# Kernel optimization log

Hardware: AMD Instinct MI355X
Metric: run time of the kernel (lower is better)

## Reference

```python
import jax, jax.numpy as jnp
import numpy as np

NUM_HEADS = 16


def rotate_half(x):
    half = x.shape[-1] // 2
    return jnp.concatenate((-x[..., half:], x[..., :half]), axis=-1)


def rope_tables(seq_len, head_dim, dtype=jnp.float32):
    inv_freq = 1.0 / (10000.0 ** (jnp.arange(0, head_dim, 2, dtype=jnp.float32) / head_dim))
    t = jnp.arange(seq_len, dtype=jnp.float32)
    freqs = jnp.outer(t, inv_freq)                 # [S, hd/2]
    emb = jnp.concatenate((freqs, freqs), axis=-1)  # [S, hd]
    return jnp.cos(emb).astype(dtype), jnp.sin(emb).astype(dtype)


def setup_inputs() -> dict:
    key = jax.random.key(0)
    k1, k2, k3 = jax.random.split(key, 3)
    B, S, D = 2, 2048, 1024
    x = jax.random.normal(k1, (B, S, D), dtype=jnp.float32)
    # causal lower-triangular mask, broadcast over batch/heads
    mask = jnp.tril(jnp.ones((S, S), dtype=bool))[None, None, :, :]
    w_qkv = jax.random.normal(k2, (3 * D, D), dtype=jnp.float32) * (D ** -0.5)
    w_out = jax.random.normal(k3, (D, D), dtype=jnp.float32) * (D ** -0.5)
    return {"x": x, "mask": mask, "w_qkv": w_qkv, "w_out": w_out}


def reference(x, mask, w_qkv, w_out):
    B, S, D = x.shape
    H = NUM_HEADS
    hd = D // H
    scale = hd ** -0.5

    qkv = jnp.einsum('bsd,ed->bse', x, w_qkv)          # [B, S, 3D]
    q, k, v = jnp.split(qkv, 3, axis=-1)

    def split(t):
        return t.reshape(B, S, H, hd).transpose(0, 2, 1, 3)  # [B, H, S, hd]

    q, k, v = split(q), split(k), split(v)

    cos, sin = rope_tables(S, hd, x.dtype)             # [S, hd]
    cos = cos[None, None]
    sin = sin[None, None]
    q = q * cos + rotate_half(q) * sin
    k = k * cos + rotate_half(k) * sin

    attn = jnp.einsum('bhqd,bhkd->bhqk', q, k) * scale  # [B, H, S, S]
    attn = jnp.where(mask, attn, jnp.float32(-jnp.inf).astype(attn.dtype))
    attn = jax.nn.softmax(attn, axis=-1)
    out = jnp.einsum('bhqk,bhkd->bhqd', attn, v)        # [B, H, S, hd]
    out = out.transpose(0, 2, 1, 3).reshape(B, S, D)
    return jnp.einsum('bsd,ed->bse', out, w_out)
```

## Files before the change

kernel.cpp:

```cpp
#include <hip/hip_runtime.h>
#include <hip/hip_bf16.h>

typedef __attribute__((ext_vector_type(8))) __bf16 bf16x8;
typedef __attribute__((ext_vector_type(4))) __bf16 bf16x4;
typedef __attribute__((ext_vector_type(2))) __bf16 bf16x2;
typedef __attribute__((ext_vector_type(4))) float f32x4;
typedef __attribute__((ext_vector_type(16))) float f32x16;

#define SEQ 2048
#define NH 16
#define HD 64
#define DMODEL 1024
#define BATCH 2
#define MTOT 4096

__device__ __forceinline__ void gl_lds16(const void* g, void* l) {
    __builtin_amdgcn_global_load_lds(
        (const __attribute__((address_space(1))) void*)(uintptr_t)g,
        (__attribute__((address_space(3))) void*)(uintptr_t)l,
        16, 0, 0);
}

__device__ __forceinline__ unsigned pk2(float x, float y) {
    union { bf16x2 h; unsigned u; } c;
    c.h = bf16x2{ (__bf16)x, (__bf16)y };
    return c.u;
}

__global__ __launch_bounds__(256) void cast3(const float4* __restrict__ x,
                                             const float4* __restrict__ wq,
                                             const float4* __restrict__ wo,
                                             __bf16* __restrict__ xb,
                                             __bf16* __restrict__ wqb,
                                             __bf16* __restrict__ wob) {
    const int NX  = 1024 * 1024;
    const int NWQ = 768 * 1024;
    const int NTOT = NX + NWQ + 256 * 1024;
    int i = blockIdx.x * 256 + threadIdx.x;
    if (i >= NTOT) return;
    float4 v; __bf16* dst; int j;
    if (i < NX)            { j = i;            v = x[j];  dst = xb;  }
    else if (i < NX + NWQ) { j = i - NX;       v = wq[j]; dst = wqb; }
    else                   { j = i - NX - NWQ; v = wo[j]; dst = wob; }
    bf16x4 o = { (__bf16)v.x, (__bf16)v.y, (__bf16)v.z, (__bf16)v.w };
    *(bf16x4*)(dst + (size_t)j * 4) = o;
}

__global__ __launch_bounds__(256) void gemm_bt(const __bf16* __restrict__ A,
                                               const __bf16* __restrict__ Bt,
                                               __bf16* __restrict__ Cb,
                                               float* __restrict__ Cf,
                                               int M, int N, int K, int bf16out) {
    __shared__ __bf16 sA[128 * 64];
    __shared__ __bf16 sB[128 * 64];
    const int tid = threadIdx.x, lane = tid & 63, wave = tid >> 6;
    const int lrow = lane & 15, quad = lane >> 4;
    const int m0 = blockIdx.y * 128, n0 = blockIdx.x * 128;
    const int wm = wave >> 1, wn = wave & 1;

    const __bf16* ap[4]; const __bf16* bp[4]; int ldso[4];
#pragma unroll
    for (int i = 0; i < 4; ++i) {
        int r0 = i * 32 + wave * 8;
        int row = r0 + (lane >> 3);
        int cg = (lane & 7) ^ (row & 7);
        ap[i] = A + (size_t)(m0 + row) * K + cg * 8;
        bp[i] = Bt + (size_t)(n0 + row) * K + cg * 8;
        ldso[i] = r0 * 128;
    }
    int arow[4], brow[4];
#pragma unroll
    for (int i = 0; i < 4; ++i) {
        arow[i] = wm * 64 + i * 16 + lrow;
        brow[i] = wn * 64 + i * 16 + lrow;
    }

    f32x4 z = {0.f, 0.f, 0.f, 0.f};
    f32x4 acc[4][4];
#pragma unroll
    for (int i = 0; i < 4; ++i)
#pragma unroll
        for (int j = 0; j < 4; ++j) acc[i][j] = z;

    char* sAb = (char*)sA; char* sBb = (char*)sB;
    for (int k0 = 0; k0 < K; k0 += 64) {
#pragma unroll
        for (int i = 0; i < 4; ++i) gl_lds16(ap[i] + k0, sAb + ldso[i]);
#pragma unroll
        for (int i = 0; i < 4; ++i) gl_lds16(bp[i] + k0, sBb + ldso[i]);
        __syncthreads();
#pragma unroll
        for (int ks = 0; ks < 2; ++ks) {
            bf16x8 af[4], bfr[4];
#pragma unroll
            for (int i = 0; i < 4; ++i)
                af[i] = *(const bf16x8*)(sAb + arow[i] * 128 +
                                         (((ks * 4 + quad) ^ (arow[i] & 7)) << 4));
#pragma unroll
            for (int i = 0; i < 4; ++i)
                bfr[i] = *(const bf16x8*)(sBb + brow[i] * 128 +
                                          (((ks * 4 + quad) ^ (brow[i] & 7)) << 4));
#pragma unroll
            for (int i = 0; i < 4; ++i)
#pragma unroll
                for (int j = 0; j < 4; ++j)
                    acc[i][j] = __builtin_amdgcn_mfma_f32_16x16x32_bf16(
                        af[i], bfr[j], acc[i][j], 0, 0, 0);
        }
        __syncthreads();
    }
#pragma unroll
    for (int i = 0; i < 4; ++i)
#pragma unroll
        for (int j = 0; j < 4; ++j)
#pragma unroll
            for (int r = 0; r < 4; ++r) {
                int row = m0 + wm * 64 + i * 16 + quad * 4 + r;
                int col = n0 + wn * 64 + j * 16 + lrow;
                if (bf16out) Cb[(size_t)row * N + col] = (__bf16)acc[i][j][r];
                else         Cf[(size_t)row * N + col] = acc[i][j][r];
            }
}

__global__ __launch_bounds__(256) void rope_qk(const __bf16* __restrict__ qkv,
                                               __bf16* __restrict__ Qp,
                                               __bf16* __restrict__ Kp) {
    int t = blockIdx.x * 256 + threadIdx.x;
    int g = t & 3, hh = (t >> 2) & 15, isk = (t >> 6) & 1, m = t >> 7;
    int s = m & (SEQ - 1), b = m >> 11;
    const __bf16* src = qkv + (size_t)m * 3072 + isk * 1024 + hh * 64 + g * 8;
    bf16x8 v0 = *(const bf16x8*)src;
    bf16x8 v1 = *(const bf16x8*)(src + 32);
    float sf = (float)s;
    float scale = isk ? 1.0f : 0.18033688011112042f;
    float base = 0.15915494309189535f * exp2f(-(float)(g * 8) * 0.4152410118609203f);
    const float rj[8] = {1.0f, 0.7498942093324559f, 0.5623413251903491f,
                         0.4216965034285822f, 0.31622776601683794f,
                         0.23713737056616552f, 0.1778279410038923f,
                         0.13335214321633242f};
    bf16x8 o0, o1;
#pragma unroll
    for (int j = 0; j < 8; ++j) {
        float rev = sf * (base * rj[j]);
        float frac = rev - floorf(rev);
        float sn = __builtin_amdgcn_sinf(frac);
        float cs = __builtin_amdgcn_cosf(frac);
        float a = (float)v0[j], bb = (float)v1[j];
        o0[j] = (__bf16)((a * cs - bb * sn) * scale);
        o1[j] = (__bf16)((bb * cs + a * sn) * scale);
    }
    __bf16* dst = (isk ? Kp : Qp) + ((size_t)(b * NH + hh) * SEQ + s) * HD + g * 8;
    *(bf16x8*)dst = o0;
    *(bf16x8*)(dst + 32) = o1;
}

__global__ __launch_bounds__(256) void v_transpose(const __bf16* __restrict__ qkv,
                                                   __bf16* __restrict__ Vt) {
    __shared__ __bf16 t[64 * 80];
    const int tid = threadIdx.x;
    const int s0 = blockIdx.x * 64;
    const int bh = blockIdx.y;
    const int b = bh >> 4, h = bh & 15;
#pragma unroll
    for (int it = 0; it < 2; ++it) {
        int idx = tid + it * 256;
        int s = idx >> 3, c = idx & 7;
        bf16x8 v = *(const bf16x8*)(qkv + ((size_t)(b * SEQ + s0 + s)) * 3072 +
                                    2048 + h * 64 + c * 8);
#pragma unroll
        for (int j = 0; j < 8; ++j) t[s * 80 + c * 8 + j] = v[j];
    }
    __syncthreads();
    int j = tid >> 2, sc = (tid & 3) * 16;
    __align__(16) __bf16 tmp[16];
#pragma unroll
    for (int k = 0; k < 16; ++k) tmp[k] = t[(sc + k) * 80 + j];
    __bf16* dst = Vt + ((size_t)bh * HD + j) * SEQ + s0 + sc;
    *(bf16x8*)dst = *(bf16x8*)tmp;
    *(bf16x8*)(dst + 8) = *(bf16x8*)(tmp + 8);
}

__global__ __launch_bounds__(256) void flash_attn(const __bf16* __restrict__ Qp,
                                                  const __bf16* __restrict__ Kp,
                                                  const __bf16* __restrict__ Vtp,
                                                  __bf16* __restrict__ Aout) {
    __shared__ __bf16 sK[128 * 64];
    __shared__ __bf16 sV[2][64 * 64];

    const int tid = threadIdx.x, lane = tid & 63, wave = tid >> 6;
    const int ql = lane & 31, half = lane >> 5;
    const int bh = blockIdx.x;
    const int qt = 15 - blockIdx.y;
    const int b = bh >> 4, hh = bh & 15;
    const int q0 = qt * 128;
    const int qrow = q0 + wave * 32 + ql;

    bf16x8 qf[4];
    const __bf16* qb = Qp + ((size_t)bh * SEQ + qrow) * HD + half * 8;
#pragma unroll
    for (int kc = 0; kc < 4; ++kc) qf[kc] = *(const bf16x8*)(qb + kc * 16);

    const __bf16* kp[4]; int kldso[4];
    const __bf16* vp[4]; int vldso[4];
#pragma unroll
    for (int i = 0; i < 4; ++i) {
        int r0 = i * 32 + wave * 8;
        int row = r0 + (lane >> 3);
        int cg = (lane & 7) ^ (row & 7);
        kp[i] = Kp + ((size_t)bh * SEQ + row) * HD + cg * 8;
        kldso[i] = r0 * 128;
        int s = i >> 1;
        int rv0 = (i & 1) * 32 + wave * 8;
        int vrow = rv0 + (lane >> 3);
        int vcg = (lane & 7) ^ (vrow & 7);
        vp[i] = Vtp + ((size_t)bh * HD + vrow) * SEQ + s * 64 + vcg * 8;
        vldso[i] = s * 8192 + rv0 * 128;
    }

    char* sKb = (char*)sK;
    char* sVb = (char*)sV;

    f32x16 zz = {0.f};
    f32x16 o0 = zz, o1 = zz;
    float l = 0.f;

    const int nkt = qt + 1;
    for (int kt = 0; kt < nkt; ++kt) {
        const int k0 = kt * 128;
#pragma unroll
        for (int i = 0; i < 4; ++i) gl_lds16(kp[i] + (size_t)k0 * HD, sKb + kldso[i]);
#pragma unroll
        for (int i = 0; i < 4; ++i) gl_lds16(vp[i] + k0, sVb + vldso[i]);
        __syncthreads();

        const bool diag = (kt == nkt - 1);
#pragma unroll
        for (int ktl = 0; ktl < 4; ++ktl) {
            int keyl = ktl * 32 + ql;
            f32x16 st = zz;
#pragma unroll
            for (int kc = 0; kc < 4; ++kc) {
                bf16x8 kf = *(const bf16x8*)(
                    sKb + keyl * 128 + (((kc * 2 + half) ^ (keyl & 7)) << 4));
                st = __builtin_amdgcn_mfma_f32_32x32x16_bf16(kf, qf[kc], st, 0, 0, 0);
            }

#pragma unroll
            for (int g = 0; g < 4; ++g)
#pragma unroll
                for (int t = 0; t < 4; ++t) {
                    float e = exp2f(st[g * 4 + t]);
                    if (diag) {
                        int key = k0 + ktl * 32 + 8 * g + 4 * half + t;
                        if (key > qrow) e = 0.f;
                    }
                    st[g * 4 + t] = e;
                    l += e;
                }

#pragma unroll
            for (int lo = 0; lo < 2; ++lo) {
                int base = lo * 8;
                unsigned a0 = pk2(st[base + 0], st[base + 1]);
                unsigned a1 = pk2(st[base + 2], st[base + 3]);
                unsigned b0 = pk2(st[base + 4], st[base + 5]);
                unsigned b1 = pk2(st[base + 6], st[base + 7]);
                unsigned d0, d1, d2, d3;
#if __has_builtin(__builtin_amdgcn_permlane32_swap)
                {
                    auto r0 = __builtin_amdgcn_permlane32_swap(a0, b0, false, false);
                    auto r1 = __builtin_amdgcn_permlane32_swap(a1, b1, false, false);
                    d0 = r0[0]; d2 = r0[1];
                    d1 = r1[0]; d3 = r1[1];
                }
#else
                {
                    unsigned z0 = half ? a0 : b0;
                    unsigned z1 = half ? a1 : b1;
                    unsigned x0 = (unsigned)__shfl_xor((int)z0, 32, 64);
                    unsigned x1 = (unsigned)__shfl_xor((int)z1, 32, 64);
                    d0 = half ? x0 : a0;
                    d1 = half ? x1 : a1;
                    d2 = half ? b0 : x0;
                    d3 = half ? b1 : x1;
                }
#endif
                union { unsigned u[4]; bf16x8 v; } pf;
                pf.u[0] = d0; pf.u[1] = d1; pf.u[2] = d2; pf.u[3] = d3;

                int kb = ktl * 2 + lo;
                int sV_off = (kb >> 2) * 8192;
                int c = (kb & 3) * 2 + half;
                bf16x8 vf0 = *(const bf16x8*)(
                    sVb + sV_off + ql * 128 + ((c ^ (ql & 7)) << 4));
                bf16x8 vf1 = *(const bf16x8*)(
                    sVb + sV_off + (32 + ql) * 128 + ((c ^ (ql & 7)) << 4));
                o0 = __builtin_amdgcn_mfma_f32_32x32x16_bf16(vf0, pf.v, o0, 0, 0, 0);
                o1 = __builtin_amdgcn_mfma_f32_32x32x16_bf16(vf1, pf.v, o1, 0, 0, 0);
            }
        }
        __syncthreads();
    }

    l += __shfl_xor(l, 32, 64);
    float invl = 1.0f / l;
    __bf16* obase = Aout + ((size_t)b * SEQ + qrow) * DMODEL + hh * HD;
#pragma unroll
    for (int g = 0; g < 4; ++g) {
        bf16x4 w0 = { (__bf16)(o0[g * 4 + 0] * invl), (__bf16)(o0[g * 4 + 1] * invl),
                      (__bf16)(o0[g * 4 + 2] * invl), (__bf16)(o0[g * 4 + 3] * invl) };
        bf16x4 w1 = { (__bf16)(o1[g * 4 + 0] * invl), (__bf16)(o1[g * 4 + 1] * invl),
                      (__bf16)(o1[g * 4 + 2] * invl), (__bf16)(o1[g * 4 + 3] * invl) };
        *(bf16x4*)(obase + 8 * g + 4 * half) = w0;
        *(bf16x4*)(obase + 32 + 8 * g + 4 * half) = w1;
    }
}

extern "C" void kernel_launch(void* const* d_in, const int* in_sizes, int n_in,
                              void* d_out, int out_size, void* d_ws, size_t ws_size,
                              hipStream_t stream) {
    (void)in_sizes; (void)n_in; (void)out_size; (void)ws_size;
    const float* x  = (const float*)d_in[0];
    const float* wq = (const float*)d_in[2];
    const float* wo = (const float*)d_in[3];
    float* out = (float*)d_out;

    char* w = (char*)d_ws;
    __bf16* xb   = (__bf16*)(w);
    __bf16* wqb  = (__bf16*)(w + (8ull << 20));
    __bf16* wob  = (__bf16*)(w + (14ull << 20));
    __bf16* qkvb = (__bf16*)(w + (16ull << 20));
    __bf16* Qb   = (__bf16*)(w + (40ull << 20));
    __bf16* Kb   = (__bf16*)(w + (48ull << 20));
    __bf16* Vtb  = (__bf16*)(w + (56ull << 20));
    __bf16* aob  = xb;

    cast3<<<8192, 256, 0, stream>>>((const float4*)x, (const float4*)wq,
                                    (const float4*)wo, xb, wqb, wob);
    gemm_bt<<<dim3(24, 32), 256, 0, stream>>>(xb, wqb, qkvb, nullptr,
                                              MTOT, 3072, 1024, 1);
    rope_qk<<<2048, 256, 0, stream>>>(qkvb, Qb, Kb);
    v_transpose<<<dim3(32, 32), 256, 0, stream>>>(qkvb, Vtb);
    flash_attn<<<dim3(32, 16), 256, 0, stream>>>(Qb, Kb, Vtb, aob);
    gemm_bt<<<dim3(8, 32), 256, 0, stream>>>(aob, wob, nullptr, out,
                                             MTOT, 1024, 1024, 0);
}
```

Before: 230.5 us.

## Split causal attention over KV chunks and split-K the output projection

Long causal query tiles are now split across 2–4 KV-range chunks, so the attention grid grows from 512 to 1280 blocks with more even work per block. Unnormalized partial outputs and row sums are written to workspace that reuses the dead QKV buffer, then merged by a new combine kernel. This works without max-rescaling because the kernel already accumulates without a running max. The output GEMM also gets a two-way split-K, using fp32 atomicAdd after a memset of the output. The cost is extra partial traffic, two extra launches and atomic contention.

```diff
diff --git a/kernel.cpp b/kernel.cpp
--- a/kernel.cpp
+++ b/kernel.cpp
@@ -13,6 +13,7 @@
 #define DMODEL 1024
 #define BATCH 2
 #define MTOT 4096
+#define NCH 36
 
 __device__ __forceinline__ void gl_lds16(const void* g, void* l) {
     __builtin_amdgcn_global_load_lds(
@@ -57,6 +58,9 @@
     const int lrow = lane & 15, quad = lane >> 4;
     const int m0 = blockIdx.y * 128, n0 = blockIdx.x * 128;
     const int wm = wave >> 1, wn = wave & 1;
+    const int nz = gridDim.z;
+    const int Kh = K / nz;
+    const int kbeg = blockIdx.z * Kh, kend = kbeg + Kh;
 
     const __bf16* ap[4]; const __bf16* bp[4]; int ldso[4];
 #pragma unroll
@@ -83,7 +87,7 @@
         for (int j = 0; j < 4; ++j) acc[i][j] = z;
 
     char* sAb = (char*)sA; char* sBb = (char*)sB;
-    for (int k0 = 0; k0 < K; k0 += 64) {
+    for (int k0 = kbeg; k0 < kend; k0 += 64) {
 #pragma unroll
         for (int i = 0; i < 4; ++i) gl_lds16(ap[i] + k0, sAb + ldso[i]);
 #pragma unroll
@@ -117,8 +121,9 @@
             for (int r = 0; r < 4; ++r) {
                 int row = m0 + wm * 64 + i * 16 + quad * 4 + r;
                 int col = n0 + wn * 64 + j * 16 + lrow;
-                if (bf16out) Cb[(size_t)row * N + col] = (__bf16)acc[i][j][r];
-                else         Cf[(size_t)row * N + col] = acc[i][j][r];
+                if (bf16out)      Cb[(size_t)row * N + col] = (__bf16)acc[i][j][r];
+                else if (nz > 1)  atomicAdd(&Cf[(size_t)row * N + col], acc[i][j][r]);
+                else              Cf[(size_t)row * N + col] = acc[i][j][r];
             }
 }
 
@@ -183,14 +188,24 @@
 __global__ __launch_bounds__(256) void flash_attn(const __bf16* __restrict__ Qp,
                                                   const __bf16* __restrict__ Kp,
                                                   const __bf16* __restrict__ Vtp,
-                                                  __bf16* __restrict__ Aout) {
+                                                  __bf16* __restrict__ Aout,
+                                                  __bf16* __restrict__ Opart,
+                                                  float* __restrict__ Lpart) {
     __shared__ __bf16 sK[128 * 64];
     __shared__ __bf16 sV[2][64 * 64];
 
     const int tid = threadIdx.x, lane = tid & 63, wave = tid >> 6;
     const int ql = lane & 31, half = lane >> 5;
     const int bh = blockIdx.x;
-    const int qt = 15 - blockIdx.y;
+    const int c = blockIdx.y;
+    int qt, C, ci;
+    if (c < 4)       { qt = c;                 C = 1; ci = 0; }
+    else if (c < 12) { qt = 4 + ((c - 4) >> 1); C = 2; ci = (c - 4) & 1; }
+    else if (c < 24) { int d = c - 12; qt = 8 + d / 3; C = 3; ci = d % 3; }
+    else             { int d = c - 24; qt = 12 + (d >> 2); C = 4; ci = d & 3; }
+    const int kt0 = ((qt + 1) * ci) / C;
+    const int kt1 = ((qt + 1) * (ci + 1)) / C;
+
     const int b = bh >> 4, hh = bh & 15;
     const int q0 = qt * 128;
     const int qrow = q0 + wave * 32 + ql;
@@ -224,8 +239,7 @@
     f32x16 o0 = zz, o1 = zz;
     float l = 0.f;
 
-    const int nkt = qt + 1;
-    for (int kt = 0; kt < nkt; ++kt) {
+    for (int kt = kt0; kt < kt1; ++kt) {
         const int k0 = kt * 128;
 #pragma unroll
         for (int i = 0; i < 4; ++i) gl_lds16(kp[i] + (size_t)k0 * HD, sKb + kldso[i]);
@@ -233,7 +247,7 @@
         for (int i = 0; i < 4; ++i) gl_lds16(vp[i] + k0, sVb + vldso[i]);
         __syncthreads();
 
-        const bool diag = (kt == nkt - 1);
+        const bool diag = (kt == qt);
 #pragma unroll
         for (int ktl = 0; ktl < 4; ++ktl) {
             int keyl = ktl * 32 + ql;
@@ -290,11 +304,11 @@
 
                 int kb = ktl * 2 + lo;
                 int sV_off = (kb >> 2) * 8192;
-                int c = (kb & 3) * 2 + half;
+                int cc = (kb & 3) * 2 + half;
                 bf16x8 vf0 = *(const bf16x8*)(
-                    sVb + sV_off + ql * 128 + ((c ^ (ql & 7)) << 4));
+                    sVb + sV_off + ql * 128 + ((cc ^ (ql & 7)) << 4));
                 bf16x8 vf1 = *(const bf16x8*)(
-                    sVb + sV_off + (32 + ql) * 128 + ((c ^ (ql & 7)) << 4));
+                    sVb + sV_off + (32 + ql) * 128 + ((cc ^ (ql & 7)) << 4));
                 o0 = __builtin_amdgcn_mfma_f32_32x32x16_bf16(vf0, pf.v, o0, 0, 0, 0);
                 o1 = __builtin_amdgcn_mfma_f32_32x32x16_bf16(vf1, pf.v, o1, 0, 0, 0);
             }
@@ -303,16 +317,71 @@
     }
 
     l += __shfl_xor(l, 32, 64);
+    if (C == 1) {
+        float invl = 1.0f / l;
+        __bf16* obase = Aout + ((size_t)b * SEQ + qrow) * DMODEL + hh * HD;
+#pragma unroll
+        for (int g = 0; g < 4; ++g) {
+            bf16x4 w0 = { (__bf16)(o0[g*4+0]*invl), (__bf16)(o0[g*4+1]*invl),
+                          (__bf16)(o0[g*4+2]*invl), (__bf16)(o0[g*4+3]*invl) };
+            bf16x4 w1 = { (__bf16)(o1[g*4+0]*invl), (__bf16)(o1[g*4+1]*invl),
+                          (__bf16)(o1[g*4+2]*invl), (__bf16)(o1[g*4+3]*invl) };
+            *(bf16x4*)(obase + 8 * g + 4 * half) = w0;
+            *(bf16x4*)(obase + 32 + 8 * g + 4 * half) = w1;
+        }
+    } else {
+        int cidx = c - 4;
+        __bf16* ob = Opart + ((size_t)(bh * NCH + cidx) << 13) +
+                     (wave * 32 + ql) * 64;
+#pragma unroll
+        for (int g = 0; g < 4; ++g) {
+            bf16x4 w0 = { (__bf16)o0[g*4+0], (__bf16)o0[g*4+1],
+                          (__bf16)o0[g*4+2], (__bf16)o0[g*4+3] };
+            bf16x4 w1 = { (__bf16)o1[g*4+0], (__bf16)o1[g*4+1],
+                          (__bf16)o1[g*4+2], (__bf16)o1[g*4+3] };
+            *(bf16x4*)(ob + 8 * g + 4 * half) = w0;
+            *(bf16x4*)(ob + 32 + 8 * g + 4 * half) = w1;
+        }
+        if (!half)
+            Lpart[(bh * NCH + cidx) * 128 + wave * 32 + ql] = l;
+    }
+}
+
+__global__ __launch_bounds__(256) void combine(const __bf16* __restrict__ Opart,
+                                               const float* __restrict__ Lpart,
+                                               __bf16* __restrict__ Aout) {
+    const int bh = blockIdx.x, qt = 4 + blockIdx.y;
+    const int C = (qt + 4) >> 2;
+    const int cbase = (qt < 8) ? (qt - 4) * 2
+                     : (qt < 12) ? 8 + (qt - 8) * 3
+                                 : 20 + (qt - 12) * 4;
+    const int t = threadIdx.x;
+    const int row = t >> 1, hcol = (t & 1) * 32;
+    float acc[32];
+#pragma unroll
+    for (int i = 0; i < 32; ++i) acc[i] = 0.f;
+    float l = 0.f;
+    for (int ci = 0; ci < C; ++ci) {
+        int ch = bh * NCH + cbase + ci;
+        l += Lpart[ch * 128 + row];
+        const __bf16* p = Opart + ((size_t)ch << 13) + row * 64 + hcol;
+#pragma unroll
+        for (int k4 = 0; k4 < 4; ++k4) {
+            bf16x8 v = ((const bf16x8*)p)[k4];
+#pragma unroll
+            for (int j = 0; j < 8; ++j) acc[k4 * 8 + j] += (float)v[j];
+        }
+    }
     float invl = 1.0f / l;
-    __bf16* obase = Aout + ((size_t)b * SEQ + qrow) * DMODEL + hh * HD;
-#pragma unroll
-    for (int g = 0; g < 4; ++g) {
-        bf16x4 w0 = { (__bf16)(o0[g * 4 + 0] * invl), (__bf16)(o0[g * 4 + 1] * invl),
-                      (__bf16)(o0[g * 4 + 2] * invl), (__bf16)(o0[g * 4 + 3] * invl) };
-        bf16x4 w1 = { (__bf16)(o1[g * 4 + 0] * invl), (__bf16)(o1[g * 4 + 1] * invl),
-                      (__bf16)(o1[g * 4 + 2] * invl), (__bf16)(o1[g * 4 + 3] * invl) };
-        *(bf16x4*)(obase + 8 * g + 4 * half) = w0;
-        *(bf16x4*)(obase + 32 + 8 * g + 4 * half) = w1;
+    const int b = bh >> 4, hh = bh & 15;
+    __bf16* dst = Aout + ((size_t)(b * SEQ + qt * 128 + row)) * DMODEL +
+                  hh * 64 + hcol;
+#pragma unroll
+    for (int k4 = 0; k4 < 4; ++k4) {
+        bf16x8 w;
+#pragma unroll
+        for (int j = 0; j < 8; ++j) w[j] = (__bf16)(acc[k4 * 8 + j] * invl);
+        ((bf16x8*)dst)[k4] = w;
     }
 }
 
@@ -330,6 +399,8 @@
     __bf16* wqb  = (__bf16*)(w + (8ull << 20));
     __bf16* wob  = (__bf16*)(w + (14ull << 20));
     __bf16* qkvb = (__bf16*)(w + (16ull << 20));
+    __bf16* Opart= (__bf16*)(w + (16ull << 20));
+    float*  Lpart= (float*) (w + (35ull << 20));
     __bf16* Qb   = (__bf16*)(w + (40ull << 20));
     __bf16* Kb   = (__bf16*)(w + (48ull << 20));
     __bf16* Vtb  = (__bf16*)(w + (56ull << 20));
@@ -337,11 +408,13 @@
 
     cast3<<<8192, 256, 0, stream>>>((const float4*)x, (const float4*)wq,
                                     (const float4*)wo, xb, wqb, wob);
-    gemm_bt<<<dim3(24, 32), 256, 0, stream>>>(xb, wqb, qkvb, nullptr,
-                                              MTOT, 3072, 1024, 1);
+    gemm_bt<<<dim3(24, 32, 1), 256, 0, stream>>>(xb, wqb, qkvb, nullptr,
+                                                 MTOT, 3072, 1024, 1);
     rope_qk<<<2048, 256, 0, stream>>>(qkvb, Qb, Kb);
     v_transpose<<<dim3(32, 32), 256, 0, stream>>>(qkvb, Vtb);
-    flash_attn<<<dim3(32, 16), 256, 0, stream>>>(Qb, Kb, Vtb, aob);
-    gemm_bt<<<dim3(8, 32), 256, 0, stream>>>(aob, wob, nullptr, out,
-                                             MTOT, 1024, 1024, 0);
-}
+    flash_attn<<<dim3(32, 40), 256, 0, stream>>>(Qb, Kb, Vtb, aob, Opart, Lpart);
+    combine<<<dim3(32, 12), 256, 0, stream>>>(Opart, Lpart, aob);
+    hipMemsetAsync(out, 0, (size_t)MTOT * DMODEL * 4, stream);
+    gemm_bt<<<dim3(8, 32, 2), 256, 0, stream>>>(aob, wob, nullptr, out,
+                                                MTOT, 1024, 1024, 0);
+}
```

Measured after the change: 235.1 us. About the same (+2.0%).
